# Kernel optimization log

Measured on AMD Instinct MI355X. Metric: run time of the kernel, lower is better.

## Reference

```python
import jax, jax.numpy as jnp
import numpy as np

N_NODES = 100000


def setup_inputs() -> dict:
    key = jax.random.key(0)
    ks = jax.random.split(key, 8)
    E = 1600000
    x = jax.random.normal(ks[0], (N_NODES, 128), dtype=jnp.float32)
    src = jax.random.randint(ks[1], (E,), 0, N_NODES, dtype=jnp.int32)
    dst = jax.random.randint(ks[2], (E,), 0, N_NODES, dtype=jnp.int32)
    s = 1.0 / np.sqrt(128.0)
    w_self = jax.random.normal(ks[3], (5, 128, 128), dtype=jnp.float32) * s
    w_neigh = jax.random.normal(ks[4], (5, 128, 128), dtype=jnp.float32) * s
    b = jnp.zeros((5, 128), dtype=jnp.float32)
    w_self_out = jax.random.normal(ks[5], (128, 47), dtype=jnp.float32) * s
    w_neigh_out = jax.random.normal(ks[6], (128, 47), dtype=jnp.float32) * s
    b_out = jnp.zeros((47,), dtype=jnp.float32)
    return {"x": x, "src": src, "dst": dst, "w_self": w_self, "w_neigh": w_neigh,
            "b": b, "w_self_out": w_self_out, "w_neigh_out": w_neigh_out, "b_out": b_out}


def _mean_agg(h, src, dst, inv_deg):
    # segment-sum of source features into destination nodes, then mean
    summed = jax.ops.segment_sum(h[src], dst, num_segments=N_NODES)  # [N, d]
    return summed * inv_deg[:, None]


def _sage_layer(h, src, dst, inv_deg, ws, wn, bias):
    neigh = _mean_agg(h, src, dst, inv_deg)
    return h @ ws + neigh @ wn + bias


def reference(x, src, dst, w_self, w_neigh, b, w_self_out, w_neigh_out, b_out):
    # in-degree, clamped to 1 for isolated nodes (DGL mean aggregator behavior)
    deg = jax.ops.segment_sum(jnp.ones_like(dst, dtype=x.dtype), dst, num_segments=N_NODES)
    inv_deg = 1.0 / jnp.maximum(deg, 1.0)

    # layer 0: no ReLU after (matches original forward)
    h = _sage_layer(x, src, dst, inv_deg, w_self[0], w_neigh[0], b[0])
    # layers 1..4: SAGEConv + ReLU
    for i in range(1, 5):
        h = _sage_layer(h, src, dst, inv_deg, w_self[i], w_neigh[i], b[i])
        h = jax.nn.relu(h)
    # final layer: 128 -> num_classes, no activation
    h = _sage_layer(h, src, dst, inv_deg, w_self_out, w_neigh_out, b_out)
    return h
```

## Files before the change

kernel.cpp:

```cpp
#include <hip/hip_runtime.h>

typedef float f4 __attribute__((ext_vector_type(4)));
typedef float f32x4 __attribute__((ext_vector_type(4)));
typedef float f2 __attribute__((ext_vector_type(2)));
typedef short s16x8 __attribute__((ext_vector_type(8)));
typedef int i4 __attribute__((ext_vector_type(4)));

#define N_NODES 100000
#define NBUCK 196
#define NB1 256

__device__ inline unsigned short f2bf(float f) {
    unsigned int u = __builtin_bit_cast(unsigned int, f);
    u += 0x7FFFu + ((u >> 16) & 1u);
    return (unsigned short)(u >> 16);
}
__device__ inline float bflo(unsigned int v) { return __builtin_bit_cast(float, v << 16); }
__device__ inline float bfhi(unsigned int v) { return __builtin_bit_cast(float, v & 0xFFFF0000u); }

#define GLDS(gp, lp)                                                            \
    __builtin_amdgcn_global_load_lds(                                           \
        (const __attribute__((address_space(1))) void*)(gp),                    \
        (__attribute__((address_space(3))) void*)(lp), 16, 0, 0)

__device__ inline void acc8(f2& a0, f2& a1, f2& a2, f2& a3, i4 u) {
    f2 t0 = {bflo((unsigned int)u[0]), bfhi((unsigned int)u[0])};
    f2 t1 = {bflo((unsigned int)u[1]), bfhi((unsigned int)u[1])};
    f2 t2 = {bflo((unsigned int)u[2]), bfhi((unsigned int)u[2])};
    f2 t3 = {bflo((unsigned int)u[3]), bfhi((unsigned int)u[3])};
    a0 += t0; a1 += t1; a2 += t2; a3 += t3;
}


__global__ __launch_bounds__(256) void k_hist(const int* __restrict__ dst,
                                              int* __restrict__ histG, int E) {
    __shared__ int h[NBUCK];
    int tid = threadIdx.x;
    for (int i = tid; i < NBUCK; i += 256) h[i] = 0;
    __syncthreads();
    int chunk = (E + NB1 - 1) / NB1;
    int s = blockIdx.x * chunk, eN = min(E, s + chunk);
    for (int i = s + tid; i < eN; i += 256) atomicAdd(&h[dst[i] >> 9], 1);
    __syncthreads();
    for (int i = tid; i < NBUCK; i += 256) histG[i * NB1 + blockIdx.x] = h[i];
}

__global__ __launch_bounds__(1024) void k_scanB(int* __restrict__ histG) {
    __shared__ int ps[1024];
    int t = threadIdx.x;
    int base = t * 49;
    int vals[49];
    int sum = 0;
#pragma unroll
    for (int i = 0; i < 49; ++i) { vals[i] = histG[base + i]; sum += vals[i]; }
    ps[t] = sum;
    __syncthreads();
    for (int off = 1; off < 1024; off <<= 1) {
        int v = (t >= off) ? ps[t - off] : 0;
        __syncthreads();
        ps[t] += v;
        __syncthreads();
    }
    int run = ps[t] - sum;
#pragma unroll
    for (int i = 0; i < 49; ++i) { int v = vals[i]; histG[base + i] = run; run += v; }
}

__global__ __launch_bounds__(256) void k_place(const int* __restrict__ src,
                                               const int* __restrict__ dst,
                                               const int* __restrict__ histG,
                                               unsigned int* __restrict__ ebuf, int E) {
    __shared__ int cur[NBUCK];
    int tid = threadIdx.x;
    for (int i = tid; i < NBUCK; i += 256) cur[i] = histG[i * NB1 + blockIdx.x];
    __syncthreads();
    int chunk = (E + NB1 - 1) / NB1;
    int s = blockIdx.x * chunk, eN = min(E, s + chunk);
    for (int i = s + tid; i < eN; i += 256) {
        int d = dst[i];
        int b = d >> 9;
        int pos = atomicAdd(&cur[b], 1);
        ebuf[pos] = (unsigned int)src[i] | ((unsigned int)(d & 511) << 17);
    }
}

__global__ __launch_bounds__(256) void k_csr(const unsigned int* __restrict__ ebuf,
                                             const int* __restrict__ histG,
                                             int* __restrict__ rp, int* __restrict__ col,
                                             float* __restrict__ invd, int N, int E) {
    __shared__ int ldeg[512];
    __shared__ int lbase[512];
    int b = blockIdx.x, tid = threadIdx.x;
    int base = histG[b * NB1];
    int endB = (b == NBUCK - 1) ? E : histG[(b + 1) * NB1];
    int cnt = endB - base;
    int n0 = b << 9;

    ldeg[tid] = 0;
    ldeg[tid + 256] = 0;
    __syncthreads();
    for (int i = tid; i < cnt; i += 256) atomicAdd(&ldeg[ebuf[base + i] >> 17], 1);
    __syncthreads();

    int a0 = ldeg[tid], a1 = ldeg[tid + 256];
    lbase[tid] = a0;
    lbase[tid + 256] = a1;
    __syncthreads();
    for (int off = 1; off < 512; off <<= 1) {
        int v0 = (tid >= off) ? lbase[tid - off] : 0;
        int v1 = (tid + 256 >= off) ? lbase[tid + 256 - off] : 0;
        __syncthreads();
        lbase[tid] += v0;
        lbase[tid + 256] += v1;
        __syncthreads();
    }
    int e0 = lbase[tid] - a0, e1 = lbase[tid + 256] - a1;
    __syncthreads();
    lbase[tid] = e0;
    lbase[tid + 256] = e1;
    ldeg[tid] = 0;
    ldeg[tid + 256] = 0;
    __syncthreads();

    for (int i = tid; i < cnt; i += 256) {
        unsigned int p = ebuf[base + i];
        int dl = p >> 17;
        int pos = base + lbase[dl] + atomicAdd(&ldeg[dl], 1);
        col[pos] = (int)(p & 0x1FFFFu) << 8;
    }

    int g0 = n0 + tid, g1 = n0 + tid + 256;
    if (g0 < N) { rp[g0] = base + e0; invd[g0] = 1.0f / fmaxf((float)a0, 1.0f); }
    if (g1 < N) { rp[g1] = base + e1; invd[g1] = 1.0f / fmaxf((float)a1, 1.0f); }
    if (b == NBUCK - 1 && tid == 0) rp[N] = E;
    if (b == NBUCK - 1 && tid < 32) col[E + tid] = 0;
}


__global__ void k_cvt(const float* __restrict__ x, unsigned short* __restrict__ xb, int n8) {
    int t = blockIdx.x * 256 + threadIdx.x;
    if (t >= n8) return;
    f4 a = *(const f4*)&x[(size_t)t * 8];
    f4 b = *(const f4*)&x[(size_t)t * 8 + 4];
    s16x8 p;
    p[0] = (short)f2bf(a[0]); p[1] = (short)f2bf(a[1]);
    p[2] = (short)f2bf(a[2]); p[3] = (short)f2bf(a[3]);
    p[4] = (short)f2bf(b[0]); p[5] = (short)f2bf(b[1]);
    p[6] = (short)f2bf(b[2]); p[7] = (short)f2bf(b[3]);
    *(s16x8*)&xb[(size_t)t * 8] = p;
}

__global__ void k_prepw(const float* __restrict__ ws, const float* __restrict__ wn,
                        unsigned short* __restrict__ wp) {
    int t = blockIdx.x * 256 + threadIdx.x;
    if (t >= 5 * 4096) return;
    int l = t & 63, nfg = (t >> 6) & 7, ks = (t >> 9) & 7, lyr = t >> 12;
    int n = nfg * 16 + (l & 15);
    s16x8 p;
#pragma unroll
    for (int j = 0; j < 8; ++j) {
        int k = ks * 32 + (l >> 4) * 8 + j;
        float v = (k < 128) ? ws[((size_t)lyr * 128 + k) * 128 + n]
                            : wn[((size_t)lyr * 128 + (k - 128)) * 128 + n];
        p[j] = (short)f2bf(v);
    }
    *(s16x8*)&wp[(size_t)t * 8] = p;
}

__global__ void k_prepwo(const float* __restrict__ wso, const float* __restrict__ wno,
                         unsigned short* __restrict__ wS, unsigned short* __restrict__ wN,
                         const float* __restrict__ bo, float* __restrict__ bo48) {
    int t = blockIdx.x * 256 + threadIdx.x;
    if (t < 48) bo48[t] = (t < 47) ? bo[t] : 0.f;
    if (t >= 2 * 768) return;
    int tbl = t / 768, r = t % 768;
    int ks = r / 192, nf = (r / 64) % 3, l = r & 63;
    int n = nf * 16 + (l & 15);
    const float* W = tbl ? wno : wso;
    unsigned short* dstp = tbl ? wN : wS;
    s16x8 p;
#pragma unroll
    for (int j = 0; j < 8; ++j) {
        int k = ks * 32 + (l >> 4) * 8 + j;
        float v = (n < 47) ? W[(size_t)k * 47 + n] : 0.f;
        p[j] = (short)f2bf(v);
    }
    *(s16x8*)&dstp[(size_t)r * 8] = p;
}


__global__ __launch_bounds__(256) void k_agg(const unsigned short* __restrict__ h,
                                             const int* __restrict__ rp,
                                             const int* __restrict__ col,
                                             const float* __restrict__ invd,
                                             unsigned short* __restrict__ out, int n) {
    int gw = (blockIdx.x * 256 + threadIdx.x) >> 6;
    int lane = threadIdx.x & 63;
    if (gw >= n) return;
    const char* hb = (const char*)h;
    const int sub = lane >> 4;
    const int lb = (lane & 15) * 16;
    int beg = rp[gw], end = rp[gw + 1];
    f2 a0 = {0.f, 0.f}, a1 = {0.f, 0.f}, a2 = {0.f, 0.f}, a3 = {0.f, 0.f};
    int e = beg;
    for (; e + 8 <= end; e += 8) {
        unsigned int c0 = (unsigned int)col[e + sub];
        unsigned int c1 = (unsigned int)col[e + 4 + sub];
        i4 u, v;
        __builtin_memcpy(&u, hb + c0 + lb, 16);
        __builtin_memcpy(&v, hb + c1 + lb, 16);
        acc8(a0, a1, a2, a3, u);
        acc8(a0, a1, a2, a3, v);
    }
    if (e < end) {
        unsigned int c0 = (unsigned int)col[e + sub];
        unsigned int c1 = (unsigned int)col[e + 4 + sub];
        i4 u, v;
        __builtin_memcpy(&u, hb + c0 + lb, 16);
        __builtin_memcpy(&v, hb + c1 + lb, 16);
        if (e + sub < end) acc8(a0, a1, a2, a3, u);
        if (e + 4 + sub < end) acc8(a0, a1, a2, a3, v);
    }
#pragma unroll
    for (int off = 16; off <= 32; off <<= 1) {
        a0[0] += __shfl_xor(a0[0], off); a0[1] += __shfl_xor(a0[1], off);
        a1[0] += __shfl_xor(a1[0], off); a1[1] += __shfl_xor(a1[1], off);
        a2[0] += __shfl_xor(a2[0], off); a2[1] += __shfl_xor(a2[1], off);
        a3[0] += __shfl_xor(a3[0], off); a3[1] += __shfl_xor(a3[1], off);
    }
    if (lane < 16) {
        float iv = invd[gw];
        i4 r;
        r[0] = (int)((unsigned int)f2bf(a0[0] * iv) | ((unsigned int)f2bf(a0[1] * iv) << 16));
        r[1] = (int)((unsigned int)f2bf(a1[0] * iv) | ((unsigned int)f2bf(a1[1] * iv) << 16));
        r[2] = (int)((unsigned int)f2bf(a2[0] * iv) | ((unsigned int)f2bf(a2[1] * iv) << 16));
        r[3] = (int)((unsigned int)f2bf(a3[0] * iv) | ((unsigned int)f2bf(a3[1] * iv) << 16));
        *(i4*)((char*)out + (size_t)gw * 256 + lb) = r;
    }
}


__global__ __launch_bounds__(256, 4) void gemm128(const unsigned short* __restrict__ h,
                                                  const unsigned short* __restrict__ nb,
                                                  const unsigned short* __restrict__ wl,
                                                  const float* __restrict__ bias,
                                                  unsigned short* __restrict__ out,
                                                  int M, int relu) {
    __shared__ s16x8 afr[2048];
    const int tid = threadIdx.x;
    const int l = tid & 63, w = tid >> 6;
    const int r0 = blockIdx.x * 64;
    const int cg = (w * 4 + (l >> 4)) * 8;

#pragma unroll
    for (int i = 0; i < 4; ++i) {
        int r = r0 + i * 16 + (l & 15);
        if (r >= M) r = M - 1;
        GLDS(h + (size_t)r * 128 + cg, &afr[(w * 4 + i) * 64]);
        GLDS(nb + (size_t)r * 128 + cg, &afr[(16 + w * 4 + i) * 64]);
    }
    asm volatile("s_waitcnt vmcnt(0)");
    __syncthreads();

    const s16x8* wf = (const s16x8*)wl;

    f32x4 acc[4][2];
#pragma unroll
    for (int i = 0; i < 4; ++i)
#pragma unroll
        for (int j = 0; j < 2; ++j) acc[i][j] = (f32x4)0.f;

#pragma unroll
    for (int ks = 0; ks < 8; ++ks) {
        const int base = (ks < 4) ? (ks * 4) : (16 + (ks - 4) * 4);
        s16x8 ha[4], bw[2];
#pragma unroll
        for (int mf = 0; mf < 4; ++mf) ha[mf] = afr[(base + mf) * 64 + l];
#pragma unroll
        for (int nf = 0; nf < 2; ++nf) bw[nf] = wf[(ks * 8 + w * 2 + nf) * 64 + l];
#pragma unroll
        for (int mf = 0; mf < 4; ++mf)
#pragma unroll
            for (int nf = 0; nf < 2; ++nf)
                acc[mf][nf] = __builtin_amdgcn_mfma_f32_16x16x32_bf16(bw[nf], ha[mf],
                                                                      acc[mf][nf], 0, 0, 0);
    }

    f4 bv[2];
#pragma unroll
    for (int nf = 0; nf < 2; ++nf)
        bv[nf] = *(const f4*)&bias[w * 32 + nf * 16 + ((l >> 4) << 2)];

#pragma unroll
    for (int mf = 0; mf < 4; ++mf) {
        int row = r0 + mf * 16 + (l & 15);
        if (row >= M) continue;
#pragma unroll
        for (int nf = 0; nf < 2; ++nf) {
            int ncol = w * 32 + nf * 16 + ((l >> 4) << 2);
            f32x4 a = acc[mf][nf];
            float v0 = a[0] + bv[nf][0], v1 = a[1] + bv[nf][1];
            float v2 = a[2] + bv[nf][2], v3 = a[3] + bv[nf][3];
            if (relu) {
                v0 = fmaxf(v0, 0.f); v1 = fmaxf(v1, 0.f);
                v2 = fmaxf(v2, 0.f); v3 = fmaxf(v3, 0.f);
            }
            uint2 p;
            p.x = (unsigned int)f2bf(v0) | ((unsigned int)f2bf(v1) << 16);
            p.y = (unsigned int)f2bf(v2) | ((unsigned int)f2bf(v3) << 16);
            *(uint2*)(out + (size_t)row * 128 + ncol) = p;
        }
    }
}


__global__ __launch_bounds__(256, 4) void gemm_fin(const unsigned short* __restrict__ h,
                                                   const unsigned short* __restrict__ wS,
                                                   const unsigned short* __restrict__ wN,
                                                   const float* __restrict__ bo48,
                                                   unsigned short* __restrict__ tmpn,
                                                   float* __restrict__ selfo, int M) {
    __shared__ s16x8 afr[1024];
    const int tid = threadIdx.x;
    const int l = tid & 63, wv = tid >> 6;
    const int r0 = blockIdx.x * 64;
    const int cg = (wv * 4 + (l >> 4)) * 8;

#pragma unroll
    for (int i = 0; i < 4; ++i) {
        int r = r0 + i * 16 + (l & 15);
        if (r >= M) r = M - 1;
        GLDS(h + (size_t)r * 128 + cg, &afr[(wv * 4 + i) * 64]);
    }
    asm volatile("s_waitcnt vmcnt(0)");
    __syncthreads();

    const int mh = wv >> 1, sel = wv & 1;
    const s16x8* wf = (const s16x8*)(sel ? wN : wS);

    f32x4 acc[2][3];
#pragma unroll
    for (int i = 0; i < 2; ++i)
#pragma unroll
        for (int j = 0; j < 3; ++j) acc[i][j] = (f32x4)0.f;

#pragma unroll
    for (int ks = 0; ks < 4; ++ks) {
        s16x8 ha[2], bw[3];
#pragma unroll
        for (int mf = 0; mf < 2; ++mf) ha[mf] = afr[(ks * 4 + mh * 2 + mf) * 64 + l];
#pragma unroll
        for (int nf = 0; nf < 3; ++nf) bw[nf] = wf[(ks * 3 + nf) * 64 + l];
#pragma unroll
        for (int mf = 0; mf < 2; ++mf)
#pragma unroll
            for (int nf = 0; nf < 3; ++nf)
                acc[mf][nf] = __builtin_amdgcn_mfma_f32_16x16x32_bf16(bw[nf], ha[mf],
                                                                      acc[mf][nf], 0, 0, 0);
    }

#pragma unroll
    for (int mf = 0; mf < 2; ++mf) {
        int row = r0 + mh * 32 + mf * 16 + (l & 15);
        if (row >= M) continue;
#pragma unroll
        for (int nf = 0; nf < 3; ++nf) {
            int ncol = nf * 16 + ((l >> 4) << 2);
            f32x4 a = acc[mf][nf];
            if (sel == 0) {
                f4 bv = *(const f4*)&bo48[ncol];
                f4 o;
                o[0] = a[0] + bv[0]; o[1] = a[1] + bv[1];
                o[2] = a[2] + bv[2]; o[3] = a[3] + bv[3];
                *(f4*)&selfo[(size_t)row * 48 + ncol] = o;
            } else {
                uint2 p;
                p.x = (unsigned int)f2bf(a[0]) | ((unsigned int)f2bf(a[1]) << 16);
                p.y = (unsigned int)f2bf(a[2]) | ((unsigned int)f2bf(a[3]) << 16);
                *(uint2*)(tmpn + (size_t)row * 64 + ncol) = p;
            }
        }
    }
}


__global__ __launch_bounds__(256) void k_agg_fin(const unsigned short* __restrict__ z,
                                                 const float* __restrict__ selfo,
                                                 const int* __restrict__ rp,
                                                 const int* __restrict__ col,
                                                 const float* __restrict__ invd,
                                                 float* __restrict__ out, int n) {
    int gw = (blockIdx.x * 256 + threadIdx.x) >> 6;
    int lane = threadIdx.x & 63;
    if (gw >= n) return;
    const char* zb = (const char*)z;
    const int hhalf = lane >> 5;
    const int lb = (lane & 31) * 4;
    int beg = rp[gw], end = rp[gw + 1];
    f2 acc = {0.f, 0.f};
    int e = beg;
    for (; e + 8 <= end; e += 8) {
        unsigned int u[4];
#pragma unroll
        for (int j = 0; j < 4; ++j) {
            unsigned int c = (unsigned int)col[e + 2 * j + hhalf];
            u[j] = *(const unsigned int*)(zb + (c >> 1) + lb);
        }
#pragma unroll
        for (int j = 0; j < 4; ++j) { f2 v = {bflo(u[j]), bfhi(u[j])}; acc += v; }
    }
    if (e < end) {
        int rem = end - e;
        unsigned int u[4];
#pragma unroll
        for (int j = 0; j < 4; ++j) {
            unsigned int c = (unsigned int)col[e + 2 * j + hhalf];
            u[j] = *(const unsigned int*)(zb + (c >> 1) + lb);
        }
#pragma unroll
        for (int j = 0; j < 4; ++j) {
            if (2 * j + hhalf < rem) { f2 v = {bflo(u[j]), bfhi(u[j])}; acc += v; }
        }
    }
    f2 tot;
    tot[0] = acc[0] + __shfl_xor(acc[0], 32);
    tot[1] = acc[1] + __shfl_xor(acc[1], 32);
    float iv = invd[gw];
    if (lane < 24) {
        int c0 = lane * 2;
        f2 s = *(const f2*)&selfo[(size_t)gw * 48 + c0];
        out[(size_t)gw * 47 + c0] = s[0] + tot[0] * iv;
        if (c0 + 1 < 47) out[(size_t)gw * 47 + c0 + 1] = s[1] + tot[1] * iv;
    }
}


static inline char* alignp(char* p) {
    return (char*)(((size_t)p + 255) & ~(size_t)255);
}

extern "C" void kernel_launch(void* const* d_in, const int* in_sizes, int n_in,
                              void* d_out, int out_size, void* d_ws, size_t ws_size,
                              hipStream_t stream) {
    const float* x = (const float*)d_in[0];
    const int* src = (const int*)d_in[1];
    const int* dst = (const int*)d_in[2];
    const float* w_self = (const float*)d_in[3];
    const float* w_neigh = (const float*)d_in[4];
    const float* b = (const float*)d_in[5];
    const float* wso = (const float*)d_in[6];
    const float* wno = (const float*)d_in[7];
    const float* bo = (const float*)d_in[8];
    float* out = (float*)d_out;

    const int N = N_NODES;
    const int E = in_sizes[1];

    char* w = (char*)d_ws;
    unsigned short* xb = (unsigned short*)w;   w = alignp(w + (size_t)N * 128 * 2);
    unsigned short* hA = (unsigned short*)w;   w = alignp(w + (size_t)N * 128 * 2);
    unsigned short* hB = (unsigned short*)w;   w = alignp(w + (size_t)N * 128 * 2);
    unsigned short* nbuf = (unsigned short*)w; w = alignp(w + (size_t)N * 128 * 2);
    unsigned short* wp = (unsigned short*)w;   w = alignp(w + (size_t)5 * 32768 * 2);
    unsigned short* wS = (unsigned short*)w;   w = alignp(w + (size_t)768 * 8 * 2);
    unsigned short* wN = (unsigned short*)w;   w = alignp(w + (size_t)768 * 8 * 2);
    float* bo48 = (float*)w; w = alignp(w + 48 * 4);
    int* rp = (int*)w;       w = alignp(w + (size_t)(N + 4) * 4);
    int* col = (int*)w;      w = alignp(w + (size_t)(E + 32) * 4);
    int* histG = (int*)w;    w = alignp(w + (size_t)NBUCK * NB1 * 4);
    float* invd = (float*)w; w = alignp(w + (size_t)N * 4);

    unsigned int* ebuf = (unsigned int*)hB;
    unsigned short* tmpn = nbuf;

    k_hist<<<NB1, 256, 0, stream>>>(dst, histG, E);
    k_scanB<<<1, 1024, 0, stream>>>(histG);
    k_place<<<NB1, 256, 0, stream>>>(src, dst, histG, ebuf, E);
    k_csr<<<NBUCK, 256, 0, stream>>>(ebuf, histG, rp, col, invd, N, E);

    k_cvt<<<(N * 128 / 8 + 255) / 256, 256, 0, stream>>>(x, xb, N * 128 / 8);
    k_prepw<<<(5 * 4096 + 255) / 256, 256, 0, stream>>>(w_self, w_neigh, wp);
    k_prepwo<<<6, 256, 0, stream>>>(wso, wno, wS, wN, bo, bo48);

    const int aggBlocks = (N * 64 + 255) / 256;
    const int gemmBlocks = (N + 63) / 64;

    k_agg<<<aggBlocks, 256, 0, stream>>>(xb, rp, col, invd, nbuf, N);
    gemm128<<<gemmBlocks, 256, 0, stream>>>(xb, nbuf, wp, b, hA, N, 0);

    unsigned short* cur = hA;
    unsigned short* oth = hB;
    for (int lyr = 1; lyr < 5; ++lyr) {
        k_agg<<<aggBlocks, 256, 0, stream>>>(cur, rp, col, invd, nbuf, N);
        gemm128<<<gemmBlocks, 256, 0, stream>>>(cur, nbuf, wp + (size_t)lyr * 32768,
                                                b + (size_t)lyr * 128, oth, N, 1);
        unsigned short* t = cur; cur = oth; oth = t;
    }

    float* selfo = (float*)hB;
    gemm_fin<<<gemmBlocks, 256, 0, stream>>>(cur, wS, wN, bo48, tmpn, selfo, N);
    k_agg_fin<<<aggBlocks, 256, 0, stream>>>(tmpn, selfo, rp, col, invd, out, N);
}
```

Before: 550.8 us.

## Make gemm128 persistent with double-buffered LDS tiles and register-resident weights

gemm128 now launches a fixed grid of 512 blocks that loop over 64-row tiles. Each block loads its weight fragments into registers once and prefetches the next tile's activations into a second LDS buffer while computing the current one. The aim is to remove repeated weight loads and overlap global-to-LDS transfer with MFMA work. The cost is lower occupancy (launch bounds drop from 4 to 2 blocks) and a full vmcnt wait plus barrier per tile. The two weight-prep kernels are also merged into one launch.

```diff
diff --git a/kernel.cpp b/kernel.cpp
--- a/kernel.cpp
+++ b/kernel.cpp
@@ -9,6 +9,7 @@
 #define N_NODES 100000
 #define NBUCK 196
 #define NB1 256
+#define GEMM_PERSIST 512
 
 __device__ inline unsigned short f2bf(float f) {
     unsigned int u = __builtin_bit_cast(unsigned int, f);
@@ -150,30 +151,30 @@
     *(s16x8*)&xb[(size_t)t * 8] = p;
 }
 
-__global__ void k_prepw(const float* __restrict__ ws, const float* __restrict__ wn,
-                        unsigned short* __restrict__ wp) {
+__global__ void k_prep(const float* __restrict__ ws, const float* __restrict__ wn,
+                       unsigned short* __restrict__ wp,
+                       const float* __restrict__ wso, const float* __restrict__ wno,
+                       unsigned short* __restrict__ wS, unsigned short* __restrict__ wN,
+                       const float* __restrict__ bo, float* __restrict__ bo48) {
     int t = blockIdx.x * 256 + threadIdx.x;
-    if (t >= 5 * 4096) return;
-    int l = t & 63, nfg = (t >> 6) & 7, ks = (t >> 9) & 7, lyr = t >> 12;
-    int n = nfg * 16 + (l & 15);
-    s16x8 p;
-#pragma unroll
-    for (int j = 0; j < 8; ++j) {
-        int k = ks * 32 + (l >> 4) * 8 + j;
-        float v = (k < 128) ? ws[((size_t)lyr * 128 + k) * 128 + n]
-                            : wn[((size_t)lyr * 128 + (k - 128)) * 128 + n];
-        p[j] = (short)f2bf(v);
-    }
-    *(s16x8*)&wp[(size_t)t * 8] = p;
-}
-
-__global__ void k_prepwo(const float* __restrict__ wso, const float* __restrict__ wno,
-                         unsigned short* __restrict__ wS, unsigned short* __restrict__ wN,
-                         const float* __restrict__ bo, float* __restrict__ bo48) {
-    int t = blockIdx.x * 256 + threadIdx.x;
-    if (t < 48) bo48[t] = (t < 47) ? bo[t] : 0.f;
-    if (t >= 2 * 768) return;
-    int tbl = t / 768, r = t % 768;
+    if (t < 5 * 4096) {
+        int l = t & 63, nfg = (t >> 6) & 7, ks = (t >> 9) & 7, lyr = t >> 12;
+        int n = nfg * 16 + (l & 15);
+        s16x8 p;
+#pragma unroll
+        for (int j = 0; j < 8; ++j) {
+            int k = ks * 32 + (l >> 4) * 8 + j;
+            float v = (k < 128) ? ws[((size_t)lyr * 128 + k) * 128 + n]
+                                : wn[((size_t)lyr * 128 + (k - 128)) * 128 + n];
+            p[j] = (short)f2bf(v);
+        }
+        *(s16x8*)&wp[(size_t)t * 8] = p;
+        return;
+    }
+    int q = t - 5 * 4096;
+    if (q < 48) bo48[q] = (q < 47) ? bo[q] : 0.f;
+    if (q >= 2 * 768) return;
+    int tbl = q / 768, r = q % 768;
     int ks = r / 192, nf = (r / 64) % 3, l = r & 63;
     int n = nf * 16 + (l & 15);
     const float* W = tbl ? wno : wso;
@@ -240,76 +241,103 @@
 }
 
 
-__global__ __launch_bounds__(256, 4) void gemm128(const unsigned short* __restrict__ h,
+__global__ __launch_bounds__(256, 2) void gemm128(const unsigned short* __restrict__ h,
                                                   const unsigned short* __restrict__ nb,
                                                   const unsigned short* __restrict__ wl,
                                                   const float* __restrict__ bias,
                                                   unsigned short* __restrict__ out,
-                                                  int M, int relu) {
-    __shared__ s16x8 afr[2048];
+                                                  int M, int relu, int nt) {
+    __shared__ s16x8 afr[2][2048];
     const int tid = threadIdx.x;
     const int l = tid & 63, w = tid >> 6;
-    const int r0 = blockIdx.x * 64;
     const int cg = (w * 4 + (l >> 4)) * 8;
-
-#pragma unroll
-    for (int i = 0; i < 4; ++i) {
-        int r = r0 + i * 16 + (l & 15);
-        if (r >= M) r = M - 1;
-        GLDS(h + (size_t)r * 128 + cg, &afr[(w * 4 + i) * 64]);
-        GLDS(nb + (size_t)r * 128 + cg, &afr[(16 + w * 4 + i) * 64]);
-    }
-    asm volatile("s_waitcnt vmcnt(0)");
-    __syncthreads();
-
     const s16x8* wf = (const s16x8*)wl;
 
-    f32x4 acc[4][2];
-#pragma unroll
-    for (int i = 0; i < 4; ++i)
-#pragma unroll
-        for (int j = 0; j < 2; ++j) acc[i][j] = (f32x4)0.f;
-
-#pragma unroll
-    for (int ks = 0; ks < 8; ++ks) {
-        const int base = (ks < 4) ? (ks * 4) : (16 + (ks - 4) * 4);
-        s16x8 ha[4], bw[2];
-#pragma unroll
-        for (int mf = 0; mf < 4; ++mf) ha[mf] = afr[(base + mf) * 64 + l];
-#pragma unroll
-        for (int nf = 0; nf < 2; ++nf) bw[nf] = wf[(ks * 8 + w * 2 + nf) * 64 + l];
-#pragma unroll
-        for (int mf = 0; mf < 4; ++mf)
-#pragma unroll
-            for (int nf = 0; nf < 2; ++nf)
-                acc[mf][nf] = __builtin_amdgcn_mfma_f32_16x16x32_bf16(bw[nf], ha[mf],
-                                                                      acc[mf][nf], 0, 0, 0);
-    }
-
+    s16x8 bwr[8][2];
+#pragma unroll
+    for (int ks = 0; ks < 8; ++ks)
+#pragma unroll
+        for (int nf = 0; nf < 2; ++nf) bwr[ks][nf] = wf[(ks * 8 + w * 2 + nf) * 64 + l];
     f4 bv[2];
 #pragma unroll
     for (int nf = 0; nf < 2; ++nf)
         bv[nf] = *(const f4*)&bias[w * 32 + nf * 16 + ((l >> 4) << 2)];
 
-#pragma unroll
-    for (int mf = 0; mf < 4; ++mf) {
-        int row = r0 + mf * 16 + (l & 15);
-        if (row >= M) continue;
-#pragma unroll
-        for (int nf = 0; nf < 2; ++nf) {
-            int ncol = w * 32 + nf * 16 + ((l >> 4) << 2);
-            f32x4 a = acc[mf][nf];
-            float v0 = a[0] + bv[nf][0], v1 = a[1] + bv[nf][1];
-            float v2 = a[2] + bv[nf][2], v3 = a[3] + bv[nf][3];
-            if (relu) {
-                v0 = fmaxf(v0, 0.f); v1 = fmaxf(v1, 0.f);
-                v2 = fmaxf(v2, 0.f); v3 = fmaxf(v3, 0.f);
+    int t = blockIdx.x;
+    if (t >= nt) return;
+
+    {
+        const int r0 = t * 64;
+#pragma unroll
+        for (int i = 0; i < 4; ++i) {
+            int r = r0 + i * 16 + (l & 15);
+            if (r >= M) r = M - 1;
+            GLDS(h + (size_t)r * 128 + cg, &afr[0][(w * 4 + i) * 64]);
+            GLDS(nb + (size_t)r * 128 + cg, &afr[0][(16 + w * 4 + i) * 64]);
+        }
+    }
+    asm volatile("s_waitcnt vmcnt(0)");
+    __syncthreads();
+
+    int cur = 0;
+    for (; t < nt; t += GEMM_PERSIST) {
+        int tn = t + GEMM_PERSIST;
+        if (tn < nt) {
+            const int r0n = tn * 64;
+#pragma unroll
+            for (int i = 0; i < 4; ++i) {
+                int r = r0n + i * 16 + (l & 15);
+                if (r >= M) r = M - 1;
+                GLDS(h + (size_t)r * 128 + cg, &afr[cur ^ 1][(w * 4 + i) * 64]);
+                GLDS(nb + (size_t)r * 128 + cg, &afr[cur ^ 1][(16 + w * 4 + i) * 64]);
             }
-            uint2 p;
-            p.x = (unsigned int)f2bf(v0) | ((unsigned int)f2bf(v1) << 16);
-            p.y = (unsigned int)f2bf(v2) | ((unsigned int)f2bf(v3) << 16);
-            *(uint2*)(out + (size_t)row * 128 + ncol) = p;
-        }
+        }
+
+        const int r0 = t * 64;
+        f32x4 acc[4][2];
+#pragma unroll
+        for (int i = 0; i < 4; ++i)
+#pragma unroll
+            for (int j = 0; j < 2; ++j) acc[i][j] = (f32x4)0.f;
+
+#pragma unroll
+        for (int ks = 0; ks < 8; ++ks) {
+            const int base = (ks < 4) ? (ks * 4) : (16 + (ks - 4) * 4);
+            s16x8 ha[4];
+#pragma unroll
+            for (int mf = 0; mf < 4; ++mf) ha[mf] = afr[cur][(base + mf) * 64 + l];
+#pragma unroll
+            for (int mf = 0; mf < 4; ++mf)
+#pragma unroll
+                for (int nf = 0; nf < 2; ++nf)
+                    acc[mf][nf] = __builtin_amdgcn_mfma_f32_16x16x32_bf16(
+                        bwr[ks][nf], ha[mf], acc[mf][nf], 0, 0, 0);
+        }
+
+#pragma unroll
+        for (int mf = 0; mf < 4; ++mf) {
+            int row = r0 + mf * 16 + (l & 15);
+            if (row >= M) continue;
+#pragma unroll
+            for (int nf = 0; nf < 2; ++nf) {
+                int ncol = w * 32 + nf * 16 + ((l >> 4) << 2);
+                f32x4 a = acc[mf][nf];
+                float v0 = a[0] + bv[nf][0], v1 = a[1] + bv[nf][1];
+                float v2 = a[2] + bv[nf][2], v3 = a[3] + bv[nf][3];
+                if (relu) {
+                    v0 = fmaxf(v0, 0.f); v1 = fmaxf(v1, 0.f);
+                    v2 = fmaxf(v2, 0.f); v3 = fmaxf(v3, 0.f);
+                }
+                uint2 p;
+                p.x = (unsigned int)f2bf(v0) | ((unsigned int)f2bf(v1) << 16);
+                p.y = (unsigned int)f2bf(v2) | ((unsigned int)f2bf(v3) << 16);
+                *(uint2*)(out + (size_t)row * 128 + ncol) = p;
+            }
+        }
+
+        asm volatile("s_waitcnt vmcnt(0)");
+        __syncthreads();
+        cur ^= 1;
     }
 }
 
@@ -479,25 +507,26 @@
     k_csr<<<NBUCK, 256, 0, stream>>>(ebuf, histG, rp, col, invd, N, E);
 
     k_cvt<<<(N * 128 / 8 + 255) / 256, 256, 0, stream>>>(x, xb, N * 128 / 8);
-    k_prepw<<<(5 * 4096 + 255) / 256, 256, 0, stream>>>(w_self, w_neigh, wp);
-    k_prepwo<<<6, 256, 0, stream>>>(wso, wno, wS, wN, bo, bo48);
+    k_prep<<<(5 * 4096 + 1536 + 255) / 256, 256, 0, stream>>>(
+        w_self, w_neigh, wp, wso, wno, wS, wN, bo, bo48);
 
     const int aggBlocks = (N * 64 + 255) / 256;
-    const int gemmBlocks = (N + 63) / 64;
+    const int nt = (N + 63) / 64;
+    const int gemmGrid = (nt < GEMM_PERSIST) ? nt : GEMM_PERSIST;
 
     k_agg<<<aggBlocks, 256, 0, stream>>>(xb, rp, col, invd, nbuf, N);
-    gemm128<<<gemmBlocks, 256, 0, stream>>>(xb, nbuf, wp, b, hA, N, 0);
+    gemm128<<<gemmGrid, 256, 0, stream>>>(xb, nbuf, wp, b, hA, N, 0, nt);
 
     unsigned short* cur = hA;
     unsigned short* oth = hB;
     for (int lyr = 1; lyr < 5; ++lyr) {
         k_agg<<<aggBlocks, 256, 0, stream>>>(cur, rp, col, invd, nbuf, N);
-        gemm128<<<gemmBlocks, 256, 0, stream>>>(cur, nbuf, wp + (size_t)lyr * 32768,
-                                                b + (size_t)lyr * 128, oth, N, 1);
+        gemm128<<<gemmGrid, 256, 0, stream>>>(cur, nbuf, wp + (size_t)lyr * 32768,
+                                              b + (size_t)lyr * 128, oth, N, 1, nt);
         unsigned short* t = cur; cur = oth; oth = t;
     }
 
     float* selfo = (float*)hB;
-    gemm_fin<<<gemmBlocks, 256, 0, stream>>>(cur, wS, wN, bo48, tmpn, selfo, N);
+    gemm_fin<<<nt, 256, 0, stream>>>(cur, wS, wN, bo48, tmpn, selfo, N);
     k_agg_fin<<<aggBlocks, 256, 0, stream>>>(tmpn, selfo, rp, col, invd, out, N);
 }
```

Measured after the change: 537.1 us. -2.5%, faster.
